# Kernel optimization log

Hardware: AMD Instinct MI355X
Metric: run time of the kernel (lower is better)

The kernel has to match this reference:

```python
import jax, jax.numpy as jnp
import numpy as np

NEG_SLOPE_ATT = 0.2   # PyG GATConv attention LeakyReLU slope
NEG_SLOPE_ACT = 0.01  # F.leaky_relu default slope (applied after encoder)


def gat_conv(x, edge_index, W, a_src, a_dst, b, concat=True):
    """PyG-style GATConv with add_self_loops=True.
    x: [N, Fin], edge_index: [2, E] (row 0 = source j, row 1 = target i).
    W: [Fin, H*C], a_src/a_dst: [H, C], b: [H*C] (concat) or [C].
    """
    N = x.shape[0]
    H, C = a_src.shape
    h = (x @ W).reshape(N, H, C)                      # [N, H, C]
    alpha_s = jnp.einsum('nhc,hc->nh', h, a_src)      # [N, H]
    alpha_d = jnp.einsum('nhc,hc->nh', h, a_dst)      # [N, H]
    loop = jnp.arange(N, dtype=edge_index.dtype)
    src = jnp.concatenate([edge_index[0], loop])       # self loops appended
    dst = jnp.concatenate([edge_index[1], loop])
    e = jax.nn.leaky_relu(alpha_s[src] + alpha_d[dst], NEG_SLOPE_ATT)  # [E', H]
    # segment softmax over edges sharing the same target node
    m = jax.ops.segment_max(e, dst, num_segments=N)    # [N, H]
    ex = jnp.exp(e - m[dst])
    denom = jax.ops.segment_sum(ex, dst, num_segments=N)  # [N, H]
    att = ex / denom[dst]                              # [E', H]
    out = jax.ops.segment_sum(att[:, :, None] * h[src], dst, num_segments=N)  # [N, H, C]
    out = out.reshape(N, H * C) if concat else out.mean(axis=1)
    return out + b


def setup_inputs() -> dict:
    key = jax.random.key(0)
    ks = jax.random.split(key, 16)
    N, E = 50000, 800000
    in_dim, hidden, heads, out_dim, n_layers = 16, 16, 8, 3, 3
    hd = heads * hidden  # 128
    s = 0.1
    inp = {
        'x': jax.random.normal(ks[0], (N, in_dim), jnp.float32),
        'edge_index': jax.random.randint(ks[1], (2, E), 0, N, jnp.int64),
        'enc_W': jax.random.normal(ks[2], (in_dim, hd), jnp.float32) * s,
        'enc_as': jax.random.normal(ks[3], (heads, hidden), jnp.float32) * s,
        'enc_ad': jax.random.normal(ks[4], (heads, hidden), jnp.float32) * s,
        'enc_b': jnp.zeros((hd,), jnp.float32),
        'hid_W': jax.random.normal(ks[5], (n_layers, hd, hd), jnp.float32) * s,
        'hid_as': jax.random.normal(ks[6], (n_layers, heads, hidden), jnp.float32) * s,
        'hid_ad': jax.random.normal(ks[7], (n_layers, heads, hidden), jnp.float32) * s,
        'hid_b': jnp.zeros((n_layers, hd), jnp.float32),
        'dec_W': jax.random.normal(ks[8], (hd, out_dim), jnp.float32) * s,
        'dec_as': jax.random.normal(ks[9], (1, out_dim), jnp.float32) * s,
        'dec_ad': jax.random.normal(ks[10], (1, out_dim), jnp.float32) * s,
        'dec_b': jnp.zeros((out_dim,), jnp.float32),
    }
    return inp


def reference(x, edge_index, enc_W, enc_as, enc_ad, enc_b,
              hid_W, hid_as, hid_ad, hid_b, dec_W, dec_as, dec_ad, dec_b):
    h = gat_conv(x, edge_index, enc_W, enc_as, enc_ad, enc_b)
    h = jax.nn.leaky_relu(h, NEG_SLOPE_ACT)
    for i in range(hid_W.shape[0]):
        h = gat_conv(h, edge_index, hid_W[i], hid_as[i], hid_ad[i], hid_b[i])
    out = gat_conv(h, edge_index, dec_W, dec_as, dec_ad, dec_b)  # heads=1, concat
    return out
```

## Files before the change

kernel.cpp:

```cpp
#include <hip/hip_runtime.h>
#include <hip/hip_fp16.h>
#include <float.h>
#include <math.h>

#define NEG_ATT 0.2f
#define NEG_ACT 0.01f
#define BK 512
#define NBMAX 128

__device__ __forceinline__ float lrelu(float v, float s) { return v >= 0.f ? v : s * v; }

struct __align__(16) H8 { __half2 a, b, c, d; };
struct __align__(8)  H4 { __half2 x, y; };

typedef _Float16 f16;
typedef f16 f16x8 __attribute__((ext_vector_type(8)));
typedef float f32x4 __attribute__((ext_vector_type(4)));

__global__ void k_zero(int* p, int n) {
  int i = blockIdx.x * blockDim.x + threadIdx.x;
  if (i < n) p[i] = 0;
}

__global__ __launch_bounds__(1024) void k_bhist(const int* __restrict__ ei,
                                                int* __restrict__ bcnt, int E, int NB) {
  __shared__ int lc[NBMAX];
  int tid = threadIdx.x;
  if (tid < NB) lc[tid] = 0;
  __syncthreads();
  int e = blockIdx.x * 1024 + tid;
  if (e < E) atomicAdd(&lc[ei[E + e] >> 9], 1);
  __syncthreads();
  if (tid < NB && lc[tid]) atomicAdd(&bcnt[tid], lc[tid]);
}

__global__ void k_bscan(const int* __restrict__ bcnt, int* pair_start, int* bucket_start,
                        int* pair_cur, int N, int NB) {
  __shared__ int t1[128], t2[128];
  int tid = threadIdx.x;
  int c = (tid < NB) ? bcnt[tid] : 0;
  int nodesb = 0;
  if (tid < NB) {
    int base = tid * BK;
    nodesb = (N - base < BK) ? (N - base) : BK;
  }
  t1[tid] = c;
  t2[tid] = c + nodesb;
  __syncthreads();
  for (int off = 1; off < 128; off <<= 1) {
    int a = (tid >= off) ? t1[tid - off] : 0;
    int b = (tid >= off) ? t2[tid - off] : 0;
    __syncthreads();
    t1[tid] += a; t2[tid] += b;
    __syncthreads();
  }
  if (tid < NB) {
    int ps = t1[tid] - c, bs = t2[tid] - (c + nodesb);
    pair_start[tid] = ps;
    pair_cur[tid] = ps;
    bucket_start[tid] = bs;
  }
  if (tid == 127) {
    pair_start[NB] = t1[127];
    bucket_start[NB] = t2[127];
  }
}

__global__ __launch_bounds__(1024) void k_bappend(const int* __restrict__ ei,
                                                  int* __restrict__ pair_cur,
                                                  int* __restrict__ pairs, int E, int NB) {
  __shared__ int lc[NBMAX], lb[NBMAX];
  int tid = threadIdx.x;
  if (tid < NB) lc[tid] = 0;
  __syncthreads();
  int e = blockIdx.x * 1024 + tid;
  int b = 0, r = 0, s = 0, d = 0;
  bool valid = e < E;
  if (valid) {
    s = ei[e]; d = ei[E + e]; b = d >> 9;
    r = atomicAdd(&lc[b], 1);
  }
  __syncthreads();
  if (tid < NB && lc[tid]) lb[tid] = atomicAdd(&pair_cur[tid], lc[tid]);
  __syncthreads();
  if (valid) pairs[lb[b] + r] = s | ((d & (BK - 1)) << 17);
}

__global__ __launch_bounds__(1024) void k_bbuild(const int* __restrict__ pairs,
    const int* __restrict__ pair_start, const int* __restrict__ bucket_start,
    int* __restrict__ row_ptr, int* __restrict__ colb, int N, int NB) {
  __shared__ int deg[BK], tmp[1024], cur[BK];
  int b = blockIdx.x, tid = threadIdx.x;
  int base = b * BK;
  int nodesb = (N - base < BK) ? (N - base) : BK;
  if (tid < BK) deg[tid] = (tid < nodesb) ? 1 : 0;
  __syncthreads();
  int p0 = pair_start[b], p1 = pair_start[b + 1];
  for (int p = p0 + tid; p < p1; p += 1024)
    atomicAdd(&deg[pairs[p] >> 17], 1);
  __syncthreads();
  int v = (tid < BK) ? deg[tid] : 0;
  tmp[tid] = v;
  __syncthreads();
  for (int off = 1; off < 1024; off <<= 1) {
    int t = (tid >= off) ? tmp[tid - off] : 0;
    __syncthreads();
    tmp[tid] += t;
    __syncthreads();
  }
  int bs = bucket_start[b];
  if (tid < nodesb) {
    int ex = tmp[tid] - v;
    row_ptr[base + tid] = bs + ex;
    colb[bs + ex] = base + tid;
    cur[tid] = ex + 1;
  }
  if (b == 0 && tid == 0) row_ptr[N] = bucket_start[NB];
  __syncthreads();
  for (int p = p0 + tid; p < p1; p += 1024) {
    int pr = pairs[p];
    int r = atomicAdd(&cur[pr >> 17], 1);
    colb[bs + r] = pr & 0x1FFFF;
  }
}

__global__ __launch_bounds__(256) void k_gemm_enc(
    const float* __restrict__ x, const float* __restrict__ W,
    const float* __restrict__ a_src, const float* __restrict__ a_dst,
    __half* __restrict__ gh, float* __restrict__ as_out, float* __restrict__ ad_out,
    int N) {
  const int K = 16, KP = 20;
  __shared__ float Wl[16 * 128];
  __shared__ float xl[64 * 20];
  int tid = threadIdx.x;
  int n0 = blockIdx.x * 64;

  for (int i = tid * 4; i < (K << 6); i += 1024) {
    int row = i >> 4;
    int c = i & 15;
    float4 v = make_float4(0.f, 0.f, 0.f, 0.f);
    if (n0 + row < N) v = *(const float4*)(x + (size_t)(n0 + row) * K + c);
    *(float4*)(xl + row * KP + c) = v;
  }
  for (int i = tid * 4; i < 2048; i += 1024)
    *(float4*)(Wl + i) = *(const float4*)(W + i);
  __syncthreads();

  int ng = tid >> 4, jg = tid & 15;
  int jlo = jg * 4, jhi = 64 + jg * 4;
  float alo[4][4] = {}, ahi[4][4] = {};
  #pragma unroll 4
  for (int kk = 0; kk < K; ++kk) {
    const float4 wlo = *(const float4*)(Wl + (kk << 7) + jlo);
    const float4 whi = *(const float4*)(Wl + (kk << 7) + jhi);
    const float* xr = xl + (ng * 4) * KP + kk;
    #pragma unroll
    for (int i = 0; i < 4; ++i) {
      float xv = xr[i * KP];
      alo[i][0] += xv * wlo.x; alo[i][1] += xv * wlo.y;
      alo[i][2] += xv * wlo.z; alo[i][3] += xv * wlo.w;
      ahi[i][0] += xv * whi.x; ahi[i][1] += xv * whi.y;
      ahi[i][2] += xv * whi.z; ahi[i][3] += xv * whi.w;
    }
  }

  int hlo = jg >> 2, hhi = 4 + (jg >> 2), off4 = (jg & 3) * 4;
  #pragma unroll
  for (int i = 0; i < 4; ++i) {
    int n = n0 + ng * 4 + i;
    if (n >= N) break;
    H4 plo = { __floats2half2_rn(alo[i][0], alo[i][1]), __floats2half2_rn(alo[i][2], alo[i][3]) };
    H4 phi = { __floats2half2_rn(ahi[i][0], ahi[i][1]), __floats2half2_rn(ahi[i][2], ahi[i][3]) };
    *(H4*)(gh + (size_t)n * 128 + jlo) = plo;
    *(H4*)(gh + (size_t)n * 128 + jhi) = phi;
    float ps_lo = 0.f, pd_lo = 0.f, ps_hi = 0.f, pd_hi = 0.f;
    #pragma unroll
    for (int t = 0; t < 4; ++t) {
      ps_lo += alo[i][t] * a_src[hlo * 16 + off4 + t];
      pd_lo += alo[i][t] * a_dst[hlo * 16 + off4 + t];
      ps_hi += ahi[i][t] * a_src[hhi * 16 + off4 + t];
      pd_hi += ahi[i][t] * a_dst[hhi * 16 + off4 + t];
    }
    ps_lo += __shfl_xor(ps_lo, 1); ps_lo += __shfl_xor(ps_lo, 2);
    pd_lo += __shfl_xor(pd_lo, 1); pd_lo += __shfl_xor(pd_lo, 2);
    ps_hi += __shfl_xor(ps_hi, 1); ps_hi += __shfl_xor(ps_hi, 2);
    pd_hi += __shfl_xor(pd_hi, 1); pd_hi += __shfl_xor(pd_hi, 2);
    if ((jg & 3) == 0) {
      as_out[n * 8 + hlo] = ps_lo; ad_out[n * 8 + hlo] = pd_lo;
      as_out[n * 8 + hhi] = ps_hi; ad_out[n * 8 + hhi] = pd_hi;
    }
  }
}

__global__ __launch_bounds__(256) void k_prep_w3(
    const float* __restrict__ W, const float* __restrict__ asrc,
    const float* __restrict__ adst, __half* __restrict__ Wt, int L) {
  int idx = blockIdx.x * 256 + threadIdx.x;
  if (idx >= L * 144 * 128) return;
  int l = idx / (144 * 128);
  int rem = idx - l * 144 * 128;
  int r = rem >> 7, k = rem & 127;
  const float* Wl = W + (size_t)l * 128 * 128;
  float v;
  if (r < 128) {
    v = Wl[k * 128 + r];
  } else {
    int h = r - 128;
    const float* a = (h < 8) ? (asrc + (size_t)l * 128) : (adst + (size_t)l * 128);
    int hh = h & 7;
    v = 0.f;
    #pragma unroll
    for (int c = 0; c < 16; ++c) v += Wl[k * 128 + hh * 16 + c] * a[hh * 16 + c];
  }
  Wt[(size_t)l * 144 * 128 + r * 128 + k] = __float2half(v);
}

__global__ __launch_bounds__(256) void k_gemm_hid_mfma(
    const __half* __restrict__ xh_g, const __half* __restrict__ Wt_g,
    __half* __restrict__ gh, float* __restrict__ as_out, float* __restrict__ ad_out,
    int N) {
  __shared__ __half xh[64][136];
  __shared__ __half wt[144][136];
  int tid = threadIdx.x;
  int n0 = blockIdx.x * 64;

  for (int i = tid; i < 1024; i += 256) {
    int row = i >> 4, c8 = (i & 15) * 8;
    float4 v = make_float4(0.f, 0.f, 0.f, 0.f);
    if (n0 + row < N) v = *(const float4*)(xh_g + (size_t)(n0 + row) * 128 + c8);
    *(float4*)(&xh[row][c8]) = v;
  }
  for (int i = tid; i < 2304; i += 256) {
    int row = i >> 4, c8 = (i & 15) * 8;
    float4 v = *(const float4*)(Wt_g + (size_t)row * 128 + c8);
    *(float4*)(&wt[row][c8]) = v;
  }
  __syncthreads();

  int wave = tid >> 6, lane = tid & 63;
  int m = lane & 15, quad = lane >> 4;
  f32x4 acc[9] = {};
  #pragma unroll
  for (int kb = 0; kb < 128; kb += 32) {
    f16x8 a = *(const f16x8*)(&xh[wave * 16 + m][kb + quad * 8]);
    #pragma unroll
    for (int t = 0; t < 9; ++t) {
      f16x8 b = *(const f16x8*)(&wt[t * 16 + m][kb + quad * 8]);
      acc[t] = __builtin_amdgcn_mfma_f32_16x16x32_f16(a, b, acc[t], 0, 0, 0);
    }
  }

  #pragma unroll
  for (int r = 0; r < 4; ++r) {
    int node = n0 + wave * 16 + quad * 4 + r;
    if (node >= N) continue;
    #pragma unroll
    for (int t = 0; t < 8; ++t)
      gh[(size_t)node * 128 + t * 16 + m] = __float2half(acc[t][r]);
    float v = acc[8][r];
    if (m < 8) as_out[node * 8 + m] = v;
    else       ad_out[node * 8 + (m - 8)] = v;
  }
}

__global__ __launch_bounds__(256) void k_agg128(
    const int* __restrict__ row_ptr, const int* __restrict__ col,
    const float* __restrict__ as, const float* __restrict__ ad,
    const __half* __restrict__ gh, const float* __restrict__ bias,
    __half* __restrict__ out, int N, int act) {
  int wid = threadIdx.x >> 6;
  int lane = threadIdx.x & 63;
  int n = blockIdx.x * 4 + wid;
  bool active = n < N;
  int nc = active ? n : 0;
  int s0 = active ? row_ptr[nc] : 0;
  int s1 = active ? row_ptr[nc + 1] : 0;

  int q = lane >> 4, l16 = lane & 15;
  int c0 = l16 * 8, hq = l16 >> 1;
  float adq = ad[nc * 8 + hq];
  const __half* gq = gh + c0;
  const float* asq = as + hq;
  float den = 0.f;
  float t0 = 0.f, t1 = 0.f, t2 = 0.f, t3 = 0.f, t4 = 0.f, t5 = 0.f, t6 = 0.f, t7 = 0.f;

  int b = s0;
  for (; b + 16 <= s1; b += 16) {
    int e0 = b + q, e1 = b + 4 + q, e2 = b + 8 + q, e3 = b + 12 + q;
    int sa = col[e0], sb = col[e1], sc = col[e2], sd = col[e3];
    float aa = asq[sa * 8], ab = asq[sb * 8], ac = asq[sc * 8], ae = asq[sd * 8];
    H8 ha = *(const H8*)(gq + (size_t)sa * 128);
    H8 hb = *(const H8*)(gq + (size_t)sb * 128);
    H8 hc = *(const H8*)(gq + (size_t)sc * 128);
    H8 hd = *(const H8*)(gq + (size_t)sd * 128);
    float wa = __expf(lrelu(aa + adq, NEG_ATT));
    float wb = __expf(lrelu(ab + adq, NEG_ATT));
    float wc = __expf(lrelu(ac + adq, NEG_ATT));
    float wd = __expf(lrelu(ae + adq, NEG_ATT));
    den += wa + wb + wc + wd;
    float2 f;
    f = __half22float2(ha.a); t0 += wa * f.x; t1 += wa * f.y;
    f = __half22float2(ha.b); t2 += wa * f.x; t3 += wa * f.y;
    f = __half22float2(ha.c); t4 += wa * f.x; t5 += wa * f.y;
    f = __half22float2(ha.d); t6 += wa * f.x; t7 += wa * f.y;
    f = __half22float2(hb.a); t0 += wb * f.x; t1 += wb * f.y;
    f = __half22float2(hb.b); t2 += wb * f.x; t3 += wb * f.y;
    f = __half22float2(hb.c); t4 += wb * f.x; t5 += wb * f.y;
    f = __half22float2(hb.d); t6 += wb * f.x; t7 += wb * f.y;
    f = __half22float2(hc.a); t0 += wc * f.x; t1 += wc * f.y;
    f = __half22float2(hc.b); t2 += wc * f.x; t3 += wc * f.y;
    f = __half22float2(hc.c); t4 += wc * f.x; t5 += wc * f.y;
    f = __half22float2(hc.d); t6 += wc * f.x; t7 += wc * f.y;
    f = __half22float2(hd.a); t0 += wd * f.x; t1 += wd * f.y;
    f = __half22float2(hd.b); t2 += wd * f.x; t3 += wd * f.y;
    f = __half22float2(hd.c); t4 += wd * f.x; t5 += wd * f.y;
    f = __half22float2(hd.d); t6 += wd * f.x; t7 += wd * f.y;
  }
  for (; b + 4 <= s1; b += 4) {
    int e0 = b + q;
    int sa = col[e0];
    float aa = asq[sa * 8];
    H8 ha = *(const H8*)(gq + (size_t)sa * 128);
    float wa = __expf(lrelu(aa + adq, NEG_ATT));
    den += wa;
    float2 f;
    f = __half22float2(ha.a); t0 += wa * f.x; t1 += wa * f.y;
    f = __half22float2(ha.b); t2 += wa * f.x; t3 += wa * f.y;
    f = __half22float2(ha.c); t4 += wa * f.x; t5 += wa * f.y;
    f = __half22float2(ha.d); t6 += wa * f.x; t7 += wa * f.y;
  }
  if (b + q < s1) {
    int e0 = b + q;
    int sa = col[e0];
    float aa = asq[sa * 8];
    H8 ha = *(const H8*)(gq + (size_t)sa * 128);
    float wa = __expf(lrelu(aa + adq, NEG_ATT));
    den += wa;
    float2 f;
    f = __half22float2(ha.a); t0 += wa * f.x; t1 += wa * f.y;
    f = __half22float2(ha.b); t2 += wa * f.x; t3 += wa * f.y;
    f = __half22float2(ha.c); t4 += wa * f.x; t5 += wa * f.y;
    f = __half22float2(ha.d); t6 += wa * f.x; t7 += wa * f.y;
  }

  den += __shfl_xor(den, 16); den += __shfl_xor(den, 32);
  t0 += __shfl_xor(t0, 16); t0 += __shfl_xor(t0, 32);
  t1 += __shfl_xor(t1, 16); t1 += __shfl_xor(t1, 32);
  t2 += __shfl_xor(t2, 16); t2 += __shfl_xor(t2, 32);
  t3 += __shfl_xor(t3, 16); t3 += __shfl_xor(t3, 32);
  t4 += __shfl_xor(t4, 16); t4 += __shfl_xor(t4, 32);
  t5 += __shfl_xor(t5, 16); t5 += __shfl_xor(t5, 32);
  t6 += __shfl_xor(t6, 16); t6 += __shfl_xor(t6, 32);
  t7 += __shfl_xor(t7, 16); t7 += __shfl_xor(t7, 32);
  if (active && q == 0) {
    float inv = 1.f / den;
    const float4 b0 = *(const float4*)(bias + c0);
    const float4 b1 = *(const float4*)(bias + c0 + 4);
    float o0 = t0 * inv + b0.x, o1 = t1 * inv + b0.y;
    float o2 = t2 * inv + b0.z, o3 = t3 * inv + b0.w;
    float o4 = t4 * inv + b1.x, o5 = t5 * inv + b1.y;
    float o6 = t6 * inv + b1.z, o7 = t7 * inv + b1.w;
    if (act) {
      o0 = lrelu(o0, NEG_ACT); o1 = lrelu(o1, NEG_ACT);
      o2 = lrelu(o2, NEG_ACT); o3 = lrelu(o3, NEG_ACT);
      o4 = lrelu(o4, NEG_ACT); o5 = lrelu(o5, NEG_ACT);
      o6 = lrelu(o6, NEG_ACT); o7 = lrelu(o7, NEG_ACT);
    }
    H8 pk = { __floats2half2_rn(o0, o1), __floats2half2_rn(o2, o3),
              __floats2half2_rn(o4, o5), __floats2half2_rn(o6, o7) };
    *(H8*)(out + (size_t)n * 128 + c0) = pk;
  }
}

__global__ __launch_bounds__(256) void k_dec_gemm(
    const __half* __restrict__ h, const float* __restrict__ Wd,
    const float* __restrict__ asd, const float* __restrict__ add,
    float4* __restrict__ g4, float* __restrict__ ad_out, int N) {
  __shared__ float Wl[384];
  int tid = threadIdx.x;
  for (int i = tid; i < 384; i += 256) Wl[i] = Wd[i];
  __syncthreads();
  int n = blockIdx.x * 256 + tid;
  if (n >= N) return;
  const __half* hr = h + (size_t)n * 128;
  float a0 = 0.f, a1 = 0.f, a2 = 0.f;
  #pragma unroll 4
  for (int k = 0; k < 128; k += 8) {
    H8 hv = *(const H8*)(hr + k);
    float f[8];
    float2 p;
    p = __half22float2(hv.a); f[0] = p.x; f[1] = p.y;
    p = __half22float2(hv.b); f[2] = p.x; f[3] = p.y;
    p = __half22float2(hv.c); f[4] = p.x; f[5] = p.y;
    p = __half22float2(hv.d); f[6] = p.x; f[7] = p.y;
    #pragma unroll
    for (int i = 0; i < 8; ++i) {
      a0 += f[i] * Wl[(k + i) * 3];
      a1 += f[i] * Wl[(k + i) * 3 + 1];
      a2 += f[i] * Wl[(k + i) * 3 + 2];
    }
  }
  float as_n = a0 * asd[0] + a1 * asd[1] + a2 * asd[2];
  g4[n] = make_float4(a0, a1, a2, as_n);
  ad_out[n] = a0 * add[0] + a1 * add[1] + a2 * add[2];
}

__global__ __launch_bounds__(256) void k_dec_agg(
    const int* __restrict__ row_ptr, const int* __restrict__ col,
    const float* __restrict__ ad, const float4* __restrict__ g4,
    const float* __restrict__ b, float* __restrict__ out, int N) {
  int n = blockIdx.x * blockDim.x + threadIdx.x;
  if (n >= N) return;
  int s0 = row_ptr[n], s1 = row_ptr[n + 1];
  float adv = ad[n];
  float den = 0.f, A0 = 0.f, A1 = 0.f, A2 = 0.f;
  int k = s0;
  for (; k + 4 <= s1; k += 4) {
    int sa = col[k], sb = col[k + 1], sc = col[k + 2], sd = col[k + 3];
    float4 v0 = g4[sa], v1 = g4[sb], v2 = g4[sc], v3 = g4[sd];
    float w0 = __expf(lrelu(v0.w + adv, NEG_ATT));
    float w1 = __expf(lrelu(v1.w + adv, NEG_ATT));
    float w2 = __expf(lrelu(v2.w + adv, NEG_ATT));
    float w3 = __expf(lrelu(v3.w + adv, NEG_ATT));
    den += w0 + w1 + w2 + w3;
    A0 += w0 * v0.x + w1 * v1.x + w2 * v2.x + w3 * v3.x;
    A1 += w0 * v0.y + w1 * v1.y + w2 * v2.y + w3 * v3.y;
    A2 += w0 * v0.z + w1 * v1.z + w2 * v2.z + w3 * v3.z;
  }
  for (; k < s1; ++k) {
    float4 v = g4[col[k]];
    float w = __expf(lrelu(v.w + adv, NEG_ATT));
    den += w;
    A0 += w * v.x; A1 += w * v.y; A2 += w * v.z;
  }
  float inv = 1.f / den;
  out[(size_t)n * 3]     = A0 * inv + b[0];
  out[(size_t)n * 3 + 1] = A1 * inv + b[1];
  out[(size_t)n * 3 + 2] = A2 * inv + b[2];
}

extern "C" void kernel_launch(void* const* d_in, const int* in_sizes, int n_in,
                              void* d_out, int out_size, void* d_ws, size_t ws_size,
                              hipStream_t stream) {
  const float* x      = (const float*)d_in[0];
  const int*   ei     = (const int*)d_in[1];
  const float* enc_W  = (const float*)d_in[2];
  const float* enc_as = (const float*)d_in[3];
  const float* enc_ad = (const float*)d_in[4];
  const float* enc_b  = (const float*)d_in[5];
  const float* hid_W  = (const float*)d_in[6];
  const float* hid_as = (const float*)d_in[7];
  const float* hid_ad = (const float*)d_in[8];
  const float* hid_b  = (const float*)d_in[9];
  const float* dec_W  = (const float*)d_in[10];
  const float* dec_as = (const float*)d_in[11];
  const float* dec_ad = (const float*)d_in[12];
  const float* dec_b  = (const float*)d_in[13];

  const int N = in_sizes[0] / 16;
  const int E = in_sizes[1] / 2;
  const int L = in_sizes[6] / (128 * 128);
  const int NB = (N + BK - 1) / BK;

  char* wbase = (char*)d_ws;
  size_t woff = 0;
  auto walloc = [&](size_t bytes, size_t align) -> void* {
    woff = (woff + align - 1) & ~(align - 1);
    void* p = wbase + woff;
    woff += bytes;
    return p;
  };
  __half* gh        = (__half*)walloc((size_t)N * 128 * 2, 16);
  __half* hh        = (__half*)walloc((size_t)N * 128 * 2, 16);
  float*  as_buf    = (float*)walloc((size_t)N * 8 * 4, 16);
  float*  ad_buf    = (float*)walloc((size_t)N * 8 * 4, 16);
  float4* g4        = (float4*)walloc((size_t)N * 16, 16);
  __half* Wt_g      = (__half*)walloc((size_t)3 * 144 * 128 * 2, 16);
  int*    row_ptr   = (int*)walloc((size_t)(N + 1) * 4, 4);
  int*    colb      = (int*)walloc((size_t)(E + N) * 4, 4);
  int*    pairs     = (int*)walloc((size_t)E * 4, 4);
  int*    bcnt      = (int*)walloc((NBMAX + 1) * 4, 4);
  int*    pair_st   = (int*)walloc((NBMAX + 1) * 4, 4);
  int*    bucket_st = (int*)walloc((NBMAX + 1) * 4, 4);
  int*    pair_cur  = (int*)walloc((NBMAX + 1) * 4, 4);

  k_zero<<<dim3(1), dim3(128), 0, stream>>>(bcnt, NB);
  k_bhist<<<dim3((E + 1023) / 1024), dim3(1024), 0, stream>>>(ei, bcnt, E, NB);
  k_bscan<<<dim3(1), dim3(128), 0, stream>>>(bcnt, pair_st, bucket_st, pair_cur, N, NB);
  k_bappend<<<dim3((E + 1023) / 1024), dim3(1024), 0, stream>>>(ei, pair_cur, pairs, E, NB);
  k_bbuild<<<dim3(NB), dim3(1024), 0, stream>>>(pairs, pair_st, bucket_st, row_ptr, colb, N, NB);

  const dim3 gGemm((N + 63) / 64), b256(256);
  const dim3 gAgg((N + 3) / 4);
  const dim3 gNode((N + 255) / 256);
  const dim3 gPrep((3 * 144 * 128 + 255) / 256);

  k_prep_w3<<<gPrep, b256, 0, stream>>>(hid_W, hid_as, hid_ad, Wt_g, L);
  k_gemm_enc<<<gGemm, b256, 0, stream>>>(x, enc_W, enc_as, enc_ad, gh, as_buf, ad_buf, N);
  k_agg128<<<gAgg, b256, 0, stream>>>(row_ptr, colb, as_buf, ad_buf, gh, enc_b, hh, N, 1);

  for (int l = 0; l < L; ++l) {
    k_gemm_hid_mfma<<<gGemm, b256, 0, stream>>>(hh, Wt_g + (size_t)l * 144 * 128,
                                                gh, as_buf, ad_buf, N);
    k_agg128<<<gAgg, b256, 0, stream>>>(row_ptr, colb, as_buf, ad_buf, gh,
                                        hid_b + (size_t)l * 128, hh, N, 0);
  }

  k_dec_gemm<<<gNode, b256, 0, stream>>>(hh, dec_W, dec_as, dec_ad, g4, ad_buf, N);
  k_dec_agg<<<gNode, b256, 0, stream>>>(row_ptr, colb, ad_buf, g4, dec_b,
                                        (float*)d_out, N);
}
```

Measured before the change: 370.8 us.

## Fuse encoder GEMM, weight prep and edge histogram; fold decoder GEMM into last aggregation

Merges the encoder GEMM, hidden-weight preparation and destination-bucket histogram into one multi-role launch. Per-block partial histograms replace global atomics and the zeroing kernel, and a wider scan kernel reduces them. The final hidden aggregation now projects its output through the decoder weights directly, which removes the separate decoder GEMM kernel and the write and re-read of the last hidden features. This cuts launch count and memory traffic, at the cost of a heavier, branchier front kernel and extra shuffle reductions in the last aggregation.

```diff
diff --git a/kernel.cpp b/kernel.cpp
--- a/kernel.cpp
+++ b/kernel.cpp
@@ -17,124 +17,59 @@
 typedef f16 f16x8 __attribute__((ext_vector_type(8)));
 typedef float f32x4 __attribute__((ext_vector_type(4)));
 
-__global__ void k_zero(int* p, int n) {
-  int i = blockIdx.x * blockDim.x + threadIdx.x;
-  if (i < n) p[i] = 0;
-}
-
-__global__ __launch_bounds__(1024) void k_bhist(const int* __restrict__ ei,
-                                                int* __restrict__ bcnt, int E, int NB) {
-  __shared__ int lc[NBMAX];
-  int tid = threadIdx.x;
-  if (tid < NB) lc[tid] = 0;
-  __syncthreads();
-  int e = blockIdx.x * 1024 + tid;
-  if (e < E) atomicAdd(&lc[ei[E + e] >> 9], 1);
-  __syncthreads();
-  if (tid < NB && lc[tid]) atomicAdd(&bcnt[tid], lc[tid]);
-}
-
-__global__ void k_bscan(const int* __restrict__ bcnt, int* pair_start, int* bucket_start,
-                        int* pair_cur, int N, int NB) {
-  __shared__ int t1[128], t2[128];
-  int tid = threadIdx.x;
-  int c = (tid < NB) ? bcnt[tid] : 0;
-  int nodesb = 0;
-  if (tid < NB) {
-    int base = tid * BK;
-    nodesb = (N - base < BK) ? (N - base) : BK;
-  }
-  t1[tid] = c;
-  t2[tid] = c + nodesb;
-  __syncthreads();
-  for (int off = 1; off < 128; off <<= 1) {
-    int a = (tid >= off) ? t1[tid - off] : 0;
-    int b = (tid >= off) ? t2[tid - off] : 0;
-    __syncthreads();
-    t1[tid] += a; t2[tid] += b;
-    __syncthreads();
-  }
-  if (tid < NB) {
-    int ps = t1[tid] - c, bs = t2[tid] - (c + nodesb);
-    pair_start[tid] = ps;
-    pair_cur[tid] = ps;
-    bucket_start[tid] = bs;
-  }
-  if (tid == 127) {
-    pair_start[NB] = t1[127];
-    bucket_start[NB] = t2[127];
-  }
-}
-
-__global__ __launch_bounds__(1024) void k_bappend(const int* __restrict__ ei,
-                                                  int* __restrict__ pair_cur,
-                                                  int* __restrict__ pairs, int E, int NB) {
-  __shared__ int lc[NBMAX], lb[NBMAX];
-  int tid = threadIdx.x;
-  if (tid < NB) lc[tid] = 0;
-  __syncthreads();
-  int e = blockIdx.x * 1024 + tid;
-  int b = 0, r = 0, s = 0, d = 0;
-  bool valid = e < E;
-  if (valid) {
-    s = ei[e]; d = ei[E + e]; b = d >> 9;
-    r = atomicAdd(&lc[b], 1);
-  }
-  __syncthreads();
-  if (tid < NB && lc[tid]) lb[tid] = atomicAdd(&pair_cur[tid], lc[tid]);
-  __syncthreads();
-  if (valid) pairs[lb[b] + r] = s | ((d & (BK - 1)) << 17);
-}
-
-__global__ __launch_bounds__(1024) void k_bbuild(const int* __restrict__ pairs,
-    const int* __restrict__ pair_start, const int* __restrict__ bucket_start,
-    int* __restrict__ row_ptr, int* __restrict__ colb, int N, int NB) {
-  __shared__ int deg[BK], tmp[1024], cur[BK];
-  int b = blockIdx.x, tid = threadIdx.x;
-  int base = b * BK;
-  int nodesb = (N - base < BK) ? (N - base) : BK;
-  if (tid < BK) deg[tid] = (tid < nodesb) ? 1 : 0;
-  __syncthreads();
-  int p0 = pair_start[b], p1 = pair_start[b + 1];
-  for (int p = p0 + tid; p < p1; p += 1024)
-    atomicAdd(&deg[pairs[p] >> 17], 1);
-  __syncthreads();
-  int v = (tid < BK) ? deg[tid] : 0;
-  tmp[tid] = v;
-  __syncthreads();
-  for (int off = 1; off < 1024; off <<= 1) {
-    int t = (tid >= off) ? tmp[tid - off] : 0;
-    __syncthreads();
-    tmp[tid] += t;
-    __syncthreads();
-  }
-  int bs = bucket_start[b];
-  if (tid < nodesb) {
-    int ex = tmp[tid] - v;
-    row_ptr[base + tid] = bs + ex;
-    colb[bs + ex] = base + tid;
-    cur[tid] = ex + 1;
-  }
-  if (b == 0 && tid == 0) row_ptr[N] = bucket_start[NB];
-  __syncthreads();
-  for (int p = p0 + tid; p < p1; p += 1024) {
-    int pr = pairs[p];
-    int r = atomicAdd(&cur[pr >> 17], 1);
-    colb[bs + r] = pr & 0x1FFFF;
-  }
-}
-
-__global__ __launch_bounds__(256) void k_gemm_enc(
+__global__ __launch_bounds__(256) void k_front(
     const float* __restrict__ x, const float* __restrict__ W,
     const float* __restrict__ a_src, const float* __restrict__ a_dst,
     __half* __restrict__ gh, float* __restrict__ as_out, float* __restrict__ ad_out,
-    int N) {
+    const float* __restrict__ hid_W, const float* __restrict__ hid_as,
+    const float* __restrict__ hid_ad, __half* __restrict__ Wt,
+    const int* __restrict__ ei, int* __restrict__ hist_part,
+    int N, int E, int L, int nbEnc, int nbPrep) {
+  __shared__ float sh[16 * 128 + 64 * 20];
+  int tid = threadIdx.x;
+  int bid = blockIdx.x;
+
+  if (bid >= nbEnc + nbPrep) {
+    int* lc = (int*)sh;
+    if (tid < NBMAX) lc[tid] = 0;
+    __syncthreads();
+    int base = (bid - nbEnc - nbPrep) * 1024;
+    #pragma unroll
+    for (int j = 0; j < 4; ++j) {
+      int e = base + j * 256 + tid;
+      if (e < E) atomicAdd(&lc[ei[E + e] >> 9], 1);
+    }
+    __syncthreads();
+    if (tid < NBMAX) hist_part[(size_t)(bid - nbEnc - nbPrep) * NBMAX + tid] = lc[tid];
+    return;
+  }
+  if (bid >= nbEnc) {
+    int idx = (bid - nbEnc) * 256 + tid;
+    if (idx < L * 144 * 128) {
+      int l = idx / (144 * 128);
+      int rem = idx - l * 144 * 128;
+      int r = rem >> 7, kk = rem & 127;
+      const float* Wl = hid_W + (size_t)l * 128 * 128;
+      float v;
+      if (r < 128) {
+        v = Wl[kk * 128 + r];
+      } else {
+        int hd = r - 128;
+        const float* a = (hd < 8) ? (hid_as + (size_t)l * 128) : (hid_ad + (size_t)l * 128);
+        int h2 = hd & 7;
+        v = 0.f;
+        #pragma unroll
+        for (int c = 0; c < 16; ++c) v += Wl[kk * 128 + h2 * 16 + c] * a[h2 * 16 + c];
+      }
+      Wt[(size_t)l * 144 * 128 + r * 128 + kk] = __float2half(v);
+    }
+    return;
+  }
+
   const int K = 16, KP = 20;
-  __shared__ float Wl[16 * 128];
-  __shared__ float xl[64 * 20];
-  int tid = threadIdx.x;
-  int n0 = blockIdx.x * 64;
-
+  float* Wl = sh;
+  float* xl = sh + 16 * 128;
+  int n0 = bid * 64;
   for (int i = tid * 4; i < (K << 6); i += 1024) {
     int row = i >> 4;
     int c = i & 15;
@@ -192,27 +127,99 @@
   }
 }
 
-__global__ __launch_bounds__(256) void k_prep_w3(
-    const float* __restrict__ W, const float* __restrict__ asrc,
-    const float* __restrict__ adst, __half* __restrict__ Wt, int L) {
-  int idx = blockIdx.x * 256 + threadIdx.x;
-  if (idx >= L * 144 * 128) return;
-  int l = idx / (144 * 128);
-  int rem = idx - l * 144 * 128;
-  int r = rem >> 7, k = rem & 127;
-  const float* Wl = W + (size_t)l * 128 * 128;
-  float v;
-  if (r < 128) {
-    v = Wl[k * 128 + r];
-  } else {
-    int h = r - 128;
-    const float* a = (h < 8) ? (asrc + (size_t)l * 128) : (adst + (size_t)l * 128);
-    int hh = h & 7;
-    v = 0.f;
-    #pragma unroll
-    for (int c = 0; c < 16; ++c) v += Wl[k * 128 + hh * 16 + c] * a[hh * 16 + c];
-  }
-  Wt[(size_t)l * 144 * 128 + r * 128 + k] = __float2half(v);
+__global__ __launch_bounds__(1024) void k_bscan2(
+    const int* __restrict__ hist_part, int nbHist,
+    int* pair_st, int* bucket_st, int* pair_cur, int N, int NB) {
+  __shared__ int part[1024];
+  __shared__ int t1[128], t2[128];
+  int tid = threadIdx.x;
+  int colp = tid & 127, rg = tid >> 7;
+  int s = 0;
+  for (int r = rg; r < nbHist; r += 8) s += hist_part[(size_t)r * NBMAX + colp];
+  part[tid] = s;
+  __syncthreads();
+  int c = 0, nodesb = 0;
+  if (tid < 128) {
+    #pragma unroll
+    for (int j = 0; j < 8; ++j) c += part[j * 128 + tid];
+    if (tid < NB) {
+      int base = tid * BK;
+      nodesb = (N - base < BK) ? (N - base) : BK;
+    }
+    t1[tid] = c;
+    t2[tid] = c + nodesb;
+  }
+  __syncthreads();
+  for (int off = 1; off < 128; off <<= 1) {
+    int a = 0, b = 0;
+    if (tid < 128 && tid >= off) { a = t1[tid - off]; b = t2[tid - off]; }
+    __syncthreads();
+    if (tid < 128) { t1[tid] += a; t2[tid] += b; }
+    __syncthreads();
+  }
+  if (tid < NB) {
+    int ps = t1[tid] - c, bs = t2[tid] - (c + nodesb);
+    pair_st[tid] = ps; pair_cur[tid] = ps; bucket_st[tid] = bs;
+  }
+  if (tid == 127) { pair_st[NB] = t1[127]; bucket_st[NB] = t2[127]; }
+}
+
+__global__ __launch_bounds__(1024) void k_bappend(const int* __restrict__ ei,
+                                                  int* __restrict__ pair_cur,
+                                                  int* __restrict__ pairs, int E, int NB) {
+  __shared__ int lc[NBMAX], lb[NBMAX];
+  int tid = threadIdx.x;
+  if (tid < NB) lc[tid] = 0;
+  __syncthreads();
+  int e = blockIdx.x * 1024 + tid;
+  int b = 0, r = 0, s = 0, d = 0;
+  bool valid = e < E;
+  if (valid) {
+    s = ei[e]; d = ei[E + e]; b = d >> 9;
+    r = atomicAdd(&lc[b], 1);
+  }
+  __syncthreads();
+  if (tid < NB && lc[tid]) lb[tid] = atomicAdd(&pair_cur[tid], lc[tid]);
+  __syncthreads();
+  if (valid) pairs[lb[b] + r] = s | ((d & (BK - 1)) << 17);
+}
+
+__global__ __launch_bounds__(1024) void k_bbuild(const int* __restrict__ pairs,
+    const int* __restrict__ pair_start, const int* __restrict__ bucket_start,
+    int* __restrict__ row_ptr, int* __restrict__ colb, int N, int NB) {
+  __shared__ int deg[BK], tmp[1024], cur[BK];
+  int b = blockIdx.x, tid = threadIdx.x;
+  int base = b * BK;
+  int nodesb = (N - base < BK) ? (N - base) : BK;
+  if (tid < BK) deg[tid] = (tid < nodesb) ? 1 : 0;
+  __syncthreads();
+  int p0 = pair_start[b], p1 = pair_start[b + 1];
+  for (int p = p0 + tid; p < p1; p += 1024)
+    atomicAdd(&deg[pairs[p] >> 17], 1);
+  __syncthreads();
+  int v = (tid < BK) ? deg[tid] : 0;
+  tmp[tid] = v;
+  __syncthreads();
+  for (int off = 1; off < 1024; off <<= 1) {
+    int t = (tid >= off) ? tmp[tid - off] : 0;
+    __syncthreads();
+    tmp[tid] += t;
+    __syncthreads();
+  }
+  int bs = bucket_start[b];
+  if (tid < nodesb) {
+    int ex = tmp[tid] - v;
+    row_ptr[base + tid] = bs + ex;
+    colb[bs + ex] = base + tid;
+    cur[tid] = ex + 1;
+  }
+  if (b == 0 && tid == 0) row_ptr[N] = bucket_start[NB];
+  __syncthreads();
+  for (int p = p0 + tid; p < p1; p += 1024) {
+    int pr = pairs[p];
+    int r = atomicAdd(&cur[pr >> 17], 1);
+    colb[bs + r] = pr & 0x1FFFF;
+  }
 }
 
 __global__ __launch_bounds__(256) void k_gemm_hid_mfma(
@@ -267,7 +274,9 @@
     const int* __restrict__ row_ptr, const int* __restrict__ col,
     const float* __restrict__ as, const float* __restrict__ ad,
     const __half* __restrict__ gh, const float* __restrict__ bias,
-    __half* __restrict__ out, int N, int act) {
+    __half* __restrict__ out, int N, int act,
+    int dec, const float* __restrict__ dWd, const float* __restrict__ dasd,
+    const float* __restrict__ dadd, float4* __restrict__ g4, float* __restrict__ adn) {
   int wid = threadIdx.x >> 6;
   int lane = threadIdx.x & 63;
   int n = blockIdx.x * 4 + wid;
@@ -352,57 +361,44 @@
   t5 += __shfl_xor(t5, 16); t5 += __shfl_xor(t5, 32);
   t6 += __shfl_xor(t6, 16); t6 += __shfl_xor(t6, 32);
   t7 += __shfl_xor(t7, 16); t7 += __shfl_xor(t7, 32);
-  if (active && q == 0) {
-    float inv = 1.f / den;
-    const float4 b0 = *(const float4*)(bias + c0);
-    const float4 b1 = *(const float4*)(bias + c0 + 4);
-    float o0 = t0 * inv + b0.x, o1 = t1 * inv + b0.y;
-    float o2 = t2 * inv + b0.z, o3 = t3 * inv + b0.w;
-    float o4 = t4 * inv + b1.x, o5 = t5 * inv + b1.y;
-    float o6 = t6 * inv + b1.z, o7 = t7 * inv + b1.w;
-    if (act) {
-      o0 = lrelu(o0, NEG_ACT); o1 = lrelu(o1, NEG_ACT);
-      o2 = lrelu(o2, NEG_ACT); o3 = lrelu(o3, NEG_ACT);
-      o4 = lrelu(o4, NEG_ACT); o5 = lrelu(o5, NEG_ACT);
-      o6 = lrelu(o6, NEG_ACT); o7 = lrelu(o7, NEG_ACT);
-    }
-    H8 pk = { __floats2half2_rn(o0, o1), __floats2half2_rn(o2, o3),
-              __floats2half2_rn(o4, o5), __floats2half2_rn(o6, o7) };
-    *(H8*)(out + (size_t)n * 128 + c0) = pk;
-  }
-}
-
-__global__ __launch_bounds__(256) void k_dec_gemm(
-    const __half* __restrict__ h, const float* __restrict__ Wd,
-    const float* __restrict__ asd, const float* __restrict__ add,
-    float4* __restrict__ g4, float* __restrict__ ad_out, int N) {
-  __shared__ float Wl[384];
-  int tid = threadIdx.x;
-  for (int i = tid; i < 384; i += 256) Wl[i] = Wd[i];
-  __syncthreads();
-  int n = blockIdx.x * 256 + tid;
-  if (n >= N) return;
-  const __half* hr = h + (size_t)n * 128;
-  float a0 = 0.f, a1 = 0.f, a2 = 0.f;
-  #pragma unroll 4
-  for (int k = 0; k < 128; k += 8) {
-    H8 hv = *(const H8*)(hr + k);
-    float f[8];
-    float2 p;
-    p = __half22float2(hv.a); f[0] = p.x; f[1] = p.y;
-    p = __half22float2(hv.b); f[2] = p.x; f[3] = p.y;
-    p = __half22float2(hv.c); f[4] = p.x; f[5] = p.y;
-    p = __half22float2(hv.d); f[6] = p.x; f[7] = p.y;
+
+  float inv = 1.f / den;
+  const float4 b0 = *(const float4*)(bias + c0);
+  const float4 b1 = *(const float4*)(bias + c0 + 4);
+  float o0 = t0 * inv + b0.x, o1 = t1 * inv + b0.y;
+  float o2 = t2 * inv + b0.z, o3 = t3 * inv + b0.w;
+  float o4 = t4 * inv + b1.x, o5 = t5 * inv + b1.y;
+  float o6 = t6 * inv + b1.z, o7 = t7 * inv + b1.w;
+  if (act) {
+    o0 = lrelu(o0, NEG_ACT); o1 = lrelu(o1, NEG_ACT);
+    o2 = lrelu(o2, NEG_ACT); o3 = lrelu(o3, NEG_ACT);
+    o4 = lrelu(o4, NEG_ACT); o5 = lrelu(o5, NEG_ACT);
+    o6 = lrelu(o6, NEG_ACT); o7 = lrelu(o7, NEG_ACT);
+  }
+  if (!dec) {
+    if (active && q == 0) {
+      H8 pk = { __floats2half2_rn(o0, o1), __floats2half2_rn(o2, o3),
+                __floats2half2_rn(o4, o5), __floats2half2_rn(o6, o7) };
+      *(H8*)(out + (size_t)n * 128 + c0) = pk;
+    }
+  } else {
+    float ov[8] = {o0, o1, o2, o3, o4, o5, o6, o7};
+    float p0 = 0.f, p1 = 0.f, p2 = 0.f;
     #pragma unroll
     for (int i = 0; i < 8; ++i) {
-      a0 += f[i] * Wl[(k + i) * 3];
-      a1 += f[i] * Wl[(k + i) * 3 + 1];
-      a2 += f[i] * Wl[(k + i) * 3 + 2];
-    }
-  }
-  float as_n = a0 * asd[0] + a1 * asd[1] + a2 * asd[2];
-  g4[n] = make_float4(a0, a1, a2, as_n);
-  ad_out[n] = a0 * add[0] + a1 * add[1] + a2 * add[2];
+      float wv0 = dWd[(c0 + i) * 3], wv1 = dWd[(c0 + i) * 3 + 1], wv2 = dWd[(c0 + i) * 3 + 2];
+      p0 += ov[i] * wv0; p1 += ov[i] * wv1; p2 += ov[i] * wv2;
+    }
+    p0 += __shfl_xor(p0, 1); p0 += __shfl_xor(p0, 2); p0 += __shfl_xor(p0, 4); p0 += __shfl_xor(p0, 8);
+    p1 += __shfl_xor(p1, 1); p1 += __shfl_xor(p1, 2); p1 += __shfl_xor(p1, 4); p1 += __shfl_xor(p1, 8);
+    p2 += __shfl_xor(p2, 1); p2 += __shfl_xor(p2, 2); p2 += __shfl_xor(p2, 4); p2 += __shfl_xor(p2, 8);
+    if (active && lane == 0) {
+      float as_n = p0 * dasd[0] + p1 * dasd[1] + p2 * dasd[2];
+      float ad_n = p0 * dadd[0] + p1 * dadd[1] + p2 * dadd[2];
+      g4[n] = make_float4(p0, p1, p2, as_n);
+      adn[n] = ad_n;
+    }
+  }
 }
 
 __global__ __launch_bounds__(256) void k_dec_agg(
@@ -470,43 +466,51 @@
     woff += bytes;
     return p;
   };
+  const int nbEnc  = (N + 63) / 64;
+  const int nbPrep = (L * 144 * 128 + 255) / 256;
+  const int nbHist = (E + 1023) / 1024;
+
   __half* gh        = (__half*)walloc((size_t)N * 128 * 2, 16);
   __half* hh        = (__half*)walloc((size_t)N * 128 * 2, 16);
   float*  as_buf    = (float*)walloc((size_t)N * 8 * 4, 16);
   float*  ad_buf    = (float*)walloc((size_t)N * 8 * 4, 16);
   float4* g4        = (float4*)walloc((size_t)N * 16, 16);
+  float*  adn       = (float*)walloc((size_t)N * 4, 16);
   __half* Wt_g      = (__half*)walloc((size_t)3 * 144 * 128 * 2, 16);
   int*    row_ptr   = (int*)walloc((size_t)(N + 1) * 4, 4);
   int*    colb      = (int*)walloc((size_t)(E + N) * 4, 4);
   int*    pairs     = (int*)walloc((size_t)E * 4, 4);
-  int*    bcnt      = (int*)walloc((NBMAX + 1) * 4, 4);
+  int*    hist_part = (int*)walloc((size_t)nbHist * NBMAX * 4, 4);
   int*    pair_st   = (int*)walloc((NBMAX + 1) * 4, 4);
   int*    bucket_st = (int*)walloc((NBMAX + 1) * 4, 4);
   int*    pair_cur  = (int*)walloc((NBMAX + 1) * 4, 4);
 
-  k_zero<<<dim3(1), dim3(128), 0, stream>>>(bcnt, NB);
-  k_bhist<<<dim3((E + 1023) / 1024), dim3(1024), 0, stream>>>(ei, bcnt, E, NB);
-  k_bscan<<<dim3(1), dim3(128), 0, stream>>>(bcnt, pair_st, bucket_st, pair_cur, N, NB);
-  k_bappend<<<dim3((E + 1023) / 1024), dim3(1024), 0, stream>>>(ei, pair_cur, pairs, E, NB);
-  k_bbuild<<<dim3(NB), dim3(1024), 0, stream>>>(pairs, pair_st, bucket_st, row_ptr, colb, N, NB);
-
-  const dim3 gGemm((N + 63) / 64), b256(256);
+  const dim3 b256(256);
+  const dim3 gFront(nbEnc + nbPrep + nbHist);
+  const dim3 gGemm(nbEnc);
   const dim3 gAgg((N + 3) / 4);
   const dim3 gNode((N + 255) / 256);
-  const dim3 gPrep((3 * 144 * 128 + 255) / 256);
-
-  k_prep_w3<<<gPrep, b256, 0, stream>>>(hid_W, hid_as, hid_ad, Wt_g, L);
-  k_gemm_enc<<<gGemm, b256, 0, stream>>>(x, enc_W, enc_as, enc_ad, gh, as_buf, ad_buf, N);
-  k_agg128<<<gAgg, b256, 0, stream>>>(row_ptr, colb, as_buf, ad_buf, gh, enc_b, hh, N, 1);
+
+  k_front<<<gFront, b256, 0, stream>>>(x, enc_W, enc_as, enc_ad, gh, as_buf, ad_buf,
+                                       hid_W, hid_as, hid_ad, Wt_g, ei, hist_part,
+                                       N, E, L, nbEnc, nbPrep);
+  k_bscan2<<<dim3(1), dim3(1024), 0, stream>>>(hist_part, nbHist, pair_st, bucket_st,
+                                               pair_cur, N, NB);
+  k_bappend<<<dim3(nbHist), dim3(1024), 0, stream>>>(ei, pair_cur, pairs, E, NB);
+  k_bbuild<<<dim3(NB), dim3(1024), 0, stream>>>(pairs, pair_st, bucket_st, row_ptr, colb, N, NB);
+
+  k_agg128<<<gAgg, b256, 0, stream>>>(row_ptr, colb, as_buf, ad_buf, gh, enc_b, hh, N, 1,
+                                      0, nullptr, nullptr, nullptr, nullptr, nullptr);
 
   for (int l = 0; l < L; ++l) {
     k_gemm_hid_mfma<<<gGemm, b256, 0, stream>>>(hh, Wt_g + (size_t)l * 144 * 128,
                                                 gh, as_buf, ad_buf, N);
+    int dec = (l == L - 1) ? 1 : 0;
     k_agg128<<<gAgg, b256, 0, stream>>>(row_ptr, colb, as_buf, ad_buf, gh,
-                                        hid_b + (size_t)l * 128, hh, N, 0);
-  }
-
-  k_dec_gemm<<<gNode, b256, 0, stream>>>(hh, dec_W, dec_as, dec_ad, g4, ad_buf, N);
-  k_dec_agg<<<gNode, b256, 0, stream>>>(row_ptr, colb, ad_buf, g4, dec_b,
+                                        hid_b + (size_t)l * 128, hh, N, 0,
+                                        dec, dec_W, dec_as, dec_ad, g4, adn);
+  }
+
+  k_dec_agg<<<gNode, b256, 0, stream>>>(row_ptr, colb, adn, g4, dec_b,
                                         (float*)d_out, N);
 }
```

Measured after the change: 357.5 us. -3.6%, faster.
